# Performance work log

Hardware: AMD Instinct MI355X
Metric: run time of the kernel (lower is better)

## Reference

```python
import jax, jax.numpy as jnp
import numpy as np

DIM = 1024
DIM_HEAD = 64
HEADS = 16
NUM_LATENTS = 64
INNER = DIM_HEAD * HEADS  # 1024


def setup_inputs() -> dict:
    key = jax.random.key(0)
    ks = jax.random.split(key, 6)
    b, m, n = 8, 4, 1024
    x = jax.random.normal(ks[0], (b, m, n, DIM), dtype=jnp.float32)
    latents = jax.random.normal(ks[1], (NUM_LATENTS, DIM), dtype=jnp.float32)
    # Linear weights stored as (in, out); no bias for q/kv, bias for out (matches nn.Linear defaults)
    Wq = jax.random.normal(ks[2], (DIM, INNER), dtype=jnp.float32) * (DIM ** -0.5)
    Wkv = jax.random.normal(ks[3], (DIM, INNER * 2), dtype=jnp.float32) * (DIM ** -0.5)
    Wout = jax.random.normal(ks[4], (INNER, DIM), dtype=jnp.float32) * (INNER ** -0.5)
    bout = jax.random.normal(ks[5], (DIM,), dtype=jnp.float32) * 0.01
    return {"x": x, "latents": latents, "Wq": Wq, "Wkv": Wkv, "Wout": Wout, "bout": bout}


def reference(x, latents, Wq, Wkv, Wout, bout):
    b, m, n, d = x.shape
    h, dh = HEADS, DIM_HEAD
    scale = dh ** -0.5

    # q from latents: [n_lat, inner] -> [h, i, dh]
    q = (latents @ Wq).reshape(NUM_LATENTS, h, dh).transpose(1, 0, 2) * scale

    # k, v from media tokens: [b, m, n, 2*inner] -> two [b, h, m, n, dh]
    kv = x @ Wkv
    k, v = jnp.split(kv, 2, axis=-1)
    k = k.reshape(b, m, n, h, dh).transpose(0, 3, 1, 2, 4)  # b h m n dh
    v = v.reshape(b, m, n, h, dh).transpose(0, 3, 1, 2, 4)

    # latent k, v: [n_lat, 2*inner] -> [h, n_lat, dh] broadcast to [b, h, m, n_lat, dh]
    lkv = latents @ Wkv
    lk, lv = jnp.split(lkv, 2, axis=-1)
    lk = jnp.broadcast_to(lk.reshape(NUM_LATENTS, h, dh).transpose(1, 0, 2)[None, :, None], (b, h, m, NUM_LATENTS, dh))
    lv = jnp.broadcast_to(lv.reshape(NUM_LATENTS, h, dh).transpose(1, 0, 2)[None, :, None], (b, h, m, NUM_LATENTS, dh))

    k = jnp.concatenate((k, lk), axis=-2)  # b h m (n + n_lat) dh
    v = jnp.concatenate((v, lv), axis=-2)

    sim = jnp.einsum('hid,bhmjd->bhmij', q, k)
    attn = jax.nn.softmax(sim, axis=-1)  # stable softmax (max-subtract internal)
    out = jnp.einsum('bhmij,bhmjd->bhmid', attn, v)  # b h m i dh
    out = out.transpose(0, 2, 3, 1, 4).reshape(b, m, NUM_LATENTS, h * dh)  # b m i inner
    return out @ Wout + bout
```

## Files before the change

### kernel.cpp

```cpp
#include <hip/hip_runtime.h>
#include <cstdint>

typedef __attribute__((ext_vector_type(8))) __bf16 bf16x8;
typedef __attribute__((ext_vector_type(4))) float f32x4;
typedef __attribute__((ext_vector_type(8))) unsigned short u16x8;
typedef __attribute__((ext_vector_type(4))) unsigned short u16x4;

__device__ __forceinline__ unsigned short f2bf(float f) {
    union { float f; unsigned u; } v; v.f = f;
    unsigned u = v.u;
    return (unsigned short)((u + 0x7FFFu + ((u >> 16) & 1u)) >> 16);
}

__device__ __forceinline__ void gload_lds16(const void* g, void* l) {
    auto gp = reinterpret_cast<__attribute__((address_space(1))) unsigned*>(
        reinterpret_cast<uintptr_t>(g));
    auto lp = reinterpret_cast<__attribute__((address_space(3))) unsigned*>(
        reinterpret_cast<uintptr_t>(l));
    __builtin_amdgcn_global_load_lds(gp, lp, 16, 0, 0);
}

__global__ __launch_bounds__(256) void cvt_kernel(const float* __restrict__ in,
                                                  unsigned short* __restrict__ out, int n4) {
    int idx = blockIdx.x * 256 + threadIdx.x;
    int stride = gridDim.x * 256;
    for (int i = idx; i < n4; i += stride) {
        float4 v = ((const float4*)in)[i];
        u16x4 o;
        o.x = f2bf(v.x); o.y = f2bf(v.y); o.z = f2bf(v.z); o.w = f2bf(v.w);
        ((u16x4*)out)[i] = o;
    }
}

__global__ __launch_bounds__(256) void transpose_cvt(const float* __restrict__ in,
                                                     unsigned short* __restrict__ out,
                                                     int R, int C) {
    __shared__ float t[32][33];
    int c0 = blockIdx.x * 32, r0 = blockIdx.y * 32;
    int tx = threadIdx.x, ty = threadIdx.y;
    for (int i = ty; i < 32; i += 8)
        t[i][tx] = in[(size_t)(r0 + i) * C + c0 + tx];
    __syncthreads();
    for (int i = ty; i < 32; i += 8)
        out[(size_t)(c0 + i) * R + r0 + tx] = f2bf(t[tx][i]);
}

__global__ __launch_bounds__(256) void gemm128p(const unsigned short* __restrict__ A,
                                                const unsigned short* __restrict__ Bt,
                                                void* __restrict__ C,
                                                const float* __restrict__ bias,
                                                int M, int N, int K, float scale, int split,
                                                int c_f32) {
    __shared__ unsigned short lds[3][2][4096];
    int ntx = N >> 7;
    int nwg = gridDim.x, bid = blockIdx.x, swz = bid;
    if ((nwg & 7) == 0) { int cpx = nwg >> 3; swz = (bid & 7) * cpx + (bid >> 3); }
    int m0 = (swz / ntx) << 7, n0 = (swz % ntx) << 7;
    int tid = threadIdx.x, lane = tid & 63, w = tid >> 6;
    int wm = w >> 1, wn = w & 1;
    int lr = lane & 15, lg = lane >> 4;
    int gq = lg ^ ((lr >> 1) & 3);
    int nkt = K >> 5;

    int arow = tid >> 2;
    int sgl = (tid & 3) ^ ((arow >> 1) & 3);
    int ra0 = m0 + arow;      if (ra0 > M - 1) ra0 = M - 1;
    int ra1 = m0 + 64 + arow; if (ra1 > M - 1) ra1 = M - 1;
    const unsigned short* a0 = A + (size_t)ra0 * K + (sgl << 3);
    const unsigned short* a1 = A + (size_t)ra1 * K + (sgl << 3);
    const unsigned short* b0 = Bt + (size_t)(n0 + arow) * K + (sgl << 3);
    const unsigned short* b1 = Bt + (size_t)(n0 + 64 + arow) * K + (sgl << 3);

    f32x4 acc[4][4] = {};

#define ST_A128(bi, kt) do { \
        gload_lds16(a0 + ((kt) << 5), &lds[bi][0][w << 9]); \
        gload_lds16(a1 + ((kt) << 5), &lds[bi][0][2048 + (w << 9)]); } while (0)
#define ST_B128(bi, kt) do { \
        gload_lds16(b0 + ((kt) << 5), &lds[bi][1][w << 9]); \
        gload_lds16(b1 + ((kt) << 5), &lds[bi][1][2048 + (w << 9)]); } while (0)

    ST_A128(0, 0); ST_B128(0, 0);
    ST_A128(1, 1); ST_B128(1, 1);

    int buf = 0;
    for (int t = 0; t < nkt; ++t) {
        asm volatile("s_waitcnt vmcnt(4)" ::: "memory");
        __builtin_amdgcn_s_barrier();
        int st = t + 2; if (st >= nkt) st = nkt - 1;
        int sbuf = buf + 2; if (sbuf >= 3) sbuf -= 3;
        ST_A128(sbuf, st);
        ST_B128(sbuf, st);
        const unsigned short* pa = &lds[buf][0][((wm << 6) + lr) * 32 + (gq << 3)];
        const unsigned short* pb = &lds[buf][1][((wn << 6) + lr) * 32 + (gq << 3)];
        bf16x8 af[4], bfr[4];
#pragma unroll
        for (int nt = 0; nt < 4; nt++) bfr[nt] = *(const bf16x8*)(pb + nt * 512);
#pragma unroll
        for (int mt = 0; mt < 4; mt++) af[mt] = *(const bf16x8*)(pa + mt * 512);
        __builtin_amdgcn_s_barrier();
        __builtin_amdgcn_s_setprio(1);
#pragma unroll
        for (int mt = 0; mt < 4; mt++)
#pragma unroll
            for (int nt = 0; nt < 4; nt++)
                acc[mt][nt] = __builtin_amdgcn_mfma_f32_16x16x32_bf16(af[mt], bfr[nt], acc[mt][nt], 0, 0, 0);
        __builtin_amdgcn_s_setprio(0);
        buf++; if (buf == 3) buf = 0;
    }
#undef ST_A128
#undef ST_B128

#pragma unroll
    for (int mt = 0; mt < 4; mt++) {
#pragma unroll
        for (int nt = 0; nt < 4; nt++) {
            int col = n0 + (wn << 6) + (nt << 4) + lr;
            float sc = (col < split) ? scale : 1.0f;
            float bv = bias ? bias[col] : 0.0f;
#pragma unroll
            for (int r = 0; r < 4; r++) {
                int row = m0 + (wm << 6) + (mt << 4) + (lg << 2) + r;
                if (row < M) {
                    float v = acc[mt][nt][r] * sc + bv;
                    if (c_f32) ((float*)C)[(size_t)row * N + col] = v;
                    else       ((unsigned short*)C)[(size_t)row * N + col] = f2bf(v);
                }
            }
        }
    }
}

__global__ __launch_bounds__(512, 2) void gemm256(const unsigned short* __restrict__ A,
                                                  const unsigned short* __restrict__ Bt,
                                                  unsigned short* __restrict__ C,
                                                  int M, int N, int K) {
    __shared__ unsigned short lds[3][2][8192];
    int nkt = K >> 5;
    int ntx = N >> 8;
    int nwg = gridDim.x, bid = blockIdx.x, swz = bid;
    if ((nwg & 7) == 0) { int cpx = nwg >> 3; swz = (bid & 7) * cpx + (bid >> 3); }
    int m0 = (swz / ntx) << 8, n0 = (swz % ntx) << 8;
    int tid = threadIdx.x, lane = tid & 63, w = tid >> 6;
    int wm = w >> 2, wn = w & 3;
    int lr = lane & 15, lg = lane >> 4;
    int gq = lg ^ ((lr >> 1) & 3);

    int srow = tid >> 2;
    int sgl = (tid & 3) ^ ((srow >> 1) & 3);
    const unsigned short* a0 = A + (size_t)(m0 + srow) * K + (sgl << 3);
    const unsigned short* a1 = A + (size_t)(m0 + 128 + srow) * K + (sgl << 3);
    const unsigned short* b0 = Bt + (size_t)(n0 + srow) * K + (sgl << 3);
    const unsigned short* b1 = Bt + (size_t)(n0 + 128 + srow) * K + (sgl << 3);

    f32x4 acc[8][4] = {};

#define STAGE_A256(bufi, kt) do { \
        gload_lds16(a0 + ((kt) << 5), &lds[bufi][0][w << 9]); \
        gload_lds16(a1 + ((kt) << 5), &lds[bufi][0][4096 + (w << 9)]); } while (0)
#define STAGE_B256(bufi, kt) do { \
        gload_lds16(b0 + ((kt) << 5), &lds[bufi][1][w << 9]); \
        gload_lds16(b1 + ((kt) << 5), &lds[bufi][1][4096 + (w << 9)]); } while (0)

    STAGE_A256(0, 0); STAGE_B256(0, 0);
    STAGE_A256(1, 1); STAGE_B256(1, 1);

    int buf = 0;
    for (int t = 0; t < nkt; ++t) {
        asm volatile("s_waitcnt vmcnt(4)" ::: "memory");
        __builtin_amdgcn_s_barrier();
        int st = t + 2; if (st >= nkt) st = nkt - 1;
        int sbuf = buf + 2; if (sbuf >= 3) sbuf -= 3;

        const unsigned short* pa = &lds[buf][0][((wm << 7) + lr) * 32 + (gq << 3)];
        const unsigned short* pb = &lds[buf][1][((wn << 6) + lr) * 32 + (gq << 3)];

        STAGE_A256(sbuf, st);
        bf16x8 bfr[4], af[4];
#pragma unroll
        for (int nt = 0; nt < 4; nt++) bfr[nt] = *(const bf16x8*)(pb + nt * 512);
#pragma unroll
        for (int mt = 0; mt < 4; mt++) af[mt] = *(const bf16x8*)(pa + mt * 512);
        __builtin_amdgcn_s_barrier();
        __builtin_amdgcn_s_setprio(1);
#pragma unroll
        for (int mt = 0; mt < 4; mt++)
#pragma unroll
            for (int nt = 0; nt < 4; nt++)
                acc[mt][nt] = __builtin_amdgcn_mfma_f32_16x16x32_bf16(af[mt], bfr[nt], acc[mt][nt], 0, 0, 0);
        __builtin_amdgcn_s_setprio(0);
        __builtin_amdgcn_s_barrier();

        STAGE_B256(sbuf, st);
        bf16x8 ag[4];
#pragma unroll
        for (int mt = 0; mt < 4; mt++) ag[mt] = *(const bf16x8*)(pa + (mt + 4) * 512);
        __builtin_amdgcn_s_barrier();
        __builtin_amdgcn_s_setprio(1);
#pragma unroll
        for (int mt = 0; mt < 4; mt++)
#pragma unroll
            for (int nt = 0; nt < 4; nt++)
                acc[mt + 4][nt] = __builtin_amdgcn_mfma_f32_16x16x32_bf16(ag[mt], bfr[nt], acc[mt + 4][nt], 0, 0, 0);
        __builtin_amdgcn_s_setprio(0);

        buf++; if (buf == 3) buf = 0;
    }
#undef STAGE_A256
#undef STAGE_B256

#pragma unroll
    for (int mt = 0; mt < 8; mt++) {
#pragma unroll
        for (int nt = 0; nt < 4; nt++) {
            int col = n0 + (wn << 6) + (nt << 4) + lr;
            size_t rbase = (size_t)(m0 + (wm << 7) + (mt << 4) + (lg << 2));
#pragma unroll
            for (int r = 0; r < 4; r++)
                C[(rbase + r) * N + col] = f2bf(acc[mt][nt][r]);
        }
    }
}

__global__ __launch_bounds__(256) void attn_kernel(const unsigned short* __restrict__ qg, int qstride,
                                                   const unsigned short* __restrict__ kvg,
                                                   const unsigned short* __restrict__ lkvg, int lstride,
                                                   unsigned short* __restrict__ og) {
    __shared__ unsigned short K_lds[64 * 72];
    __shared__ unsigned short V_lds[64 * 72];
    __shared__ unsigned short P_lds[4][16 * 72];
    int bm = blockIdx.x >> 4, h = blockIdx.x & 15;
    int tid = threadIdx.x, lane = tid & 63, w = tid >> 6;
    int lr = lane & 15, lg = lane >> 4;

    bf16x8 qf[2];
#pragma unroll
    for (int kk = 0; kk < 2; kk++)
        qf[kk] = *(const bf16x8*)(qg + (size_t)((w << 4) + lr) * qstride + (h << 6) + (kk << 5) + (lg << 3));

    f32x4 acc[4] = {};
    float m_run[4], l_run[4];
#pragma unroll
    for (int r = 0; r < 4; r++) { m_run[r] = -1e30f; l_run[r] = 0.0f; }

    int jrow = tid >> 2;
    int seg = (tid & 3) << 4;

    const unsigned short* s0 = kvg + (size_t)((bm << 10) + jrow) * 2048 + (h << 6);
    u16x8 k0 = *(const u16x8*)(s0 + seg);
    u16x8 k1 = *(const u16x8*)(s0 + seg + 8);
    u16x8 v0 = *(const u16x8*)(s0 + 1024 + seg);
    u16x8 v1 = *(const u16x8*)(s0 + 1024 + seg + 8);

    for (int t = 0; t < 17; t++) {
        *(u16x8*)(&K_lds[jrow * 72 + seg]) = k0;
        *(u16x8*)(&K_lds[jrow * 72 + seg + 8]) = k1;
#pragma unroll
        for (int c = 0; c < 8; c++) V_lds[(seg + c) * 72 + jrow] = v0[c];
#pragma unroll
        for (int c = 0; c < 8; c++) V_lds[(seg + 8 + c) * 72 + jrow] = v1[c];
        __syncthreads();

        u16x8 nk0 = k0, nk1 = k1, nv0 = v0, nv1 = v1;
        if (t < 16) {
            const unsigned short* src = (t < 15)
                ? kvg + (size_t)((bm << 10) + ((t + 1) << 6) + jrow) * 2048 + (h << 6)
                : lkvg + (size_t)jrow * lstride + (h << 6);
            nk0 = *(const u16x8*)(src + seg);
            nk1 = *(const u16x8*)(src + seg + 8);
            nv0 = *(const u16x8*)(src + 1024 + seg);
            nv1 = *(const u16x8*)(src + 1024 + seg + 8);
        }

        f32x4 s[4] = {};
#pragma unroll
        for (int jt = 0; jt < 4; jt++) {
#pragma unroll
            for (int kk = 0; kk < 2; kk++) {
                bf16x8 kf = *(const bf16x8*)(&K_lds[(size_t)((jt << 4) + lr) * 72 + (kk << 5) + (lg << 3)]);
                s[jt] = __builtin_amdgcn_mfma_f32_16x16x32_bf16(qf[kk], kf, s[jt], 0, 0, 0);
            }
        }
#pragma unroll
        for (int r = 0; r < 4; r++) {
            float mx = fmaxf(fmaxf(s[0][r], s[1][r]), fmaxf(s[2][r], s[3][r]));
            mx = fmaxf(mx, __shfl_xor(mx, 1));
            mx = fmaxf(mx, __shfl_xor(mx, 2));
            mx = fmaxf(mx, __shfl_xor(mx, 4));
            mx = fmaxf(mx, __shfl_xor(mx, 8));
            float nm = fmaxf(m_run[r], mx);
            float fct = __expf(m_run[r] - nm);
            m_run[r] = nm;
            float p0 = __expf(s[0][r] - nm);
            float p1 = __expf(s[1][r] - nm);
            float p2 = __expf(s[2][r] - nm);
            float p3 = __expf(s[3][r] - nm);
            float sum = p0 + p1 + p2 + p3;
            sum += __shfl_xor(sum, 1);
            sum += __shfl_xor(sum, 2);
            sum += __shfl_xor(sum, 4);
            sum += __shfl_xor(sum, 8);
            l_run[r] = l_run[r] * fct + sum;
#pragma unroll
            for (int dt = 0; dt < 4; dt++) acc[dt][r] *= fct;
            int prow = ((lg << 2) + r) * 72;
            P_lds[w][prow + lr]      = f2bf(p0);
            P_lds[w][prow + 16 + lr] = f2bf(p1);
            P_lds[w][prow + 32 + lr] = f2bf(p2);
            P_lds[w][prow + 48 + lr] = f2bf(p3);
        }
#pragma unroll
        for (int jkk = 0; jkk < 2; jkk++) {
            bf16x8 pf = *(const bf16x8*)(&P_lds[w][(size_t)lr * 72 + (jkk << 5) + (lg << 3)]);
#pragma unroll
            for (int dt = 0; dt < 4; dt++) {
                bf16x8 vf = *(const bf16x8*)(&V_lds[(size_t)((dt << 4) + lr) * 72 + (jkk << 5) + (lg << 3)]);
                acc[dt] = __builtin_amdgcn_mfma_f32_16x16x32_bf16(pf, vf, acc[dt], 0, 0, 0);
            }
        }
        __syncthreads();
        k0 = nk0; k1 = nk1; v0 = nv0; v1 = nv1;
    }
#pragma unroll
    for (int dt = 0; dt < 4; dt++) {
#pragma unroll
        for (int r = 0; r < 4; r++) {
            int i = (w << 4) + (lg << 2) + r;
            float v = acc[dt][r] / l_run[r];
            og[(size_t)((bm << 6) + i) * 1024 + (h << 6) + (dt << 4) + lr] = f2bf(v);
        }
    }
}

extern "C" void kernel_launch(void* const* d_in, const int* in_sizes, int n_in,
                              void* d_out, int out_size, void* d_ws, size_t ws_size,
                              hipStream_t stream) {
    const float* x       = (const float*)d_in[0];
    const float* latents = (const float*)d_in[1];
    const float* Wq      = (const float*)d_in[2];
    const float* Wkv     = (const float*)d_in[3];
    const float* Wout    = (const float*)d_in[4];
    const float* bout    = (const float*)d_in[5];
    char* ws = (char*)d_ws;
    unsigned short* xb    = (unsigned short*)(ws);
    unsigned short* kvb   = (unsigned short*)(ws + 67108864);
    unsigned short* wqkvt = (unsigned short*)(ws + 201326592);
    unsigned short* wkvt  = wqkvt + 1024 * 1024;
    unsigned short* woutt = (unsigned short*)(ws + 207618048);
    unsigned short* latb  = (unsigned short*)(ws + 209715200);
    unsigned short* qlkvb = (unsigned short*)(ws + 209846272);
    unsigned short* attnb = (unsigned short*)(ws + 210239488);

    cvt_kernel<<<2048, 256, 0, stream>>>(x, xb, 33554432 / 4);
    cvt_kernel<<<64, 256, 0, stream>>>(latents, latb, 65536 / 4);
    dim3 tb(32, 8);
    transpose_cvt<<<dim3(32, 32), tb, 0, stream>>>(Wq, wqkvt, 1024, 1024);
    transpose_cvt<<<dim3(64, 32), tb, 0, stream>>>(Wkv, wkvt, 1024, 2048);
    transpose_cvt<<<dim3(32, 32), tb, 0, stream>>>(Wout, woutt, 1024, 1024);
    gemm128p<<<24, 256, 0, stream>>>(latb, wqkvt, qlkvb, nullptr, 64, 3072, 1024, 0.125f, 1024, 0);
    gemm256<<<1024, 512, 0, stream>>>(xb, wkvt, kvb, 32768, 2048, 1024);
    attn_kernel<<<512, 256, 0, stream>>>(qlkvb, 3072, kvb, qlkvb + 1024, 3072, attnb);
    gemm128p<<<128, 256, 0, stream>>>(attnb, woutt, (void*)d_out, bout, 2048, 1024, 1024, 1.0f, 0, 1);
}
```

Baseline: 271.0 us.

## Enlarge KV projection GEMM tile to 512x256 with 128x128 per-wave tiles

Replaces the 256x256-tile KV projection GEMM with a 512x256 tile in which each of the 8 waves computes a 128x128 sub-tile, halving the grid to 512 workgroups. The aim is more reuse of each LDS fragment per MFMA and less global traffic per output. The intermediate barriers inside the K loop are dropped in this kernel and one is also removed from gemm128p. In exchange, the doubled accumulator array (64 f32x4 per thread) under launch_bounds(512,2) is likely to exceed the register budget and spill. The larger triple-buffered LDS footprint also limits occupancy to one block per CU.

```diff
diff --git a/kernel.cpp b/kernel.cpp
--- a/kernel.cpp
+++ b/kernel.cpp
@@ -98,7 +98,6 @@
         for (int nt = 0; nt < 4; nt++) bfr[nt] = *(const bf16x8*)(pb + nt * 512);
 #pragma unroll
         for (int mt = 0; mt < 4; mt++) af[mt] = *(const bf16x8*)(pa + mt * 512);
-        __builtin_amdgcn_s_barrier();
         __builtin_amdgcn_s_setprio(1);
 #pragma unroll
         for (int mt = 0; mt < 4; mt++)
@@ -131,89 +130,86 @@
     }
 }
 
-__global__ __launch_bounds__(512, 2) void gemm256(const unsigned short* __restrict__ A,
+__global__ __launch_bounds__(512, 2) void gemm512(const unsigned short* __restrict__ A,
                                                   const unsigned short* __restrict__ Bt,
                                                   unsigned short* __restrict__ C,
                                                   int M, int N, int K) {
-    __shared__ unsigned short lds[3][2][8192];
+    __shared__ unsigned short lds[3][24576];
     int nkt = K >> 5;
     int ntx = N >> 8;
     int nwg = gridDim.x, bid = blockIdx.x, swz = bid;
     if ((nwg & 7) == 0) { int cpx = nwg >> 3; swz = (bid & 7) * cpx + (bid >> 3); }
-    int m0 = (swz / ntx) << 8, n0 = (swz % ntx) << 8;
+    int m0 = (swz / ntx) << 9, n0 = (swz % ntx) << 8;
     int tid = threadIdx.x, lane = tid & 63, w = tid >> 6;
-    int wm = w >> 2, wn = w & 3;
+    int wm = w >> 1, wn = w & 1;
     int lr = lane & 15, lg = lane >> 4;
     int gq = lg ^ ((lr >> 1) & 3);
 
     int srow = tid >> 2;
     int sgl = (tid & 3) ^ ((srow >> 1) & 3);
-    const unsigned short* a0 = A + (size_t)(m0 + srow) * K + (sgl << 3);
-    const unsigned short* a1 = A + (size_t)(m0 + 128 + srow) * K + (sgl << 3);
-    const unsigned short* b0 = Bt + (size_t)(n0 + srow) * K + (sgl << 3);
-    const unsigned short* b1 = Bt + (size_t)(n0 + 128 + srow) * K + (sgl << 3);
-
-    f32x4 acc[8][4] = {};
-
-#define STAGE_A256(bufi, kt) do { \
-        gload_lds16(a0 + ((kt) << 5), &lds[bufi][0][w << 9]); \
-        gload_lds16(a1 + ((kt) << 5), &lds[bufi][0][4096 + (w << 9)]); } while (0)
-#define STAGE_B256(bufi, kt) do { \
-        gload_lds16(b0 + ((kt) << 5), &lds[bufi][1][w << 9]); \
-        gload_lds16(b1 + ((kt) << 5), &lds[bufi][1][4096 + (w << 9)]); } while (0)
-
-    STAGE_A256(0, 0); STAGE_B256(0, 0);
-    STAGE_A256(1, 1); STAGE_B256(1, 1);
+    const unsigned short* aP = A + (size_t)(m0 + srow) * K + (sgl << 3);
+    const unsigned short* bP = Bt + (size_t)(n0 + srow) * K + (sgl << 3);
+    size_t aStep = (size_t)128 * K;
+
+    f32x4 acc[8][8] = {};
+
+#define ST_P1(bi, kt) do { \
+        gload_lds16(aP + ((kt) << 5),             &lds[bi][(w << 9)]); \
+        gload_lds16(aP + aStep + ((kt) << 5),     &lds[bi][4096 + (w << 9)]); \
+        gload_lds16(aP + 2 * aStep + ((kt) << 5), &lds[bi][8192 + (w << 9)]); } while (0)
+#define ST_P2(bi, kt) do { \
+        gload_lds16(aP + 3 * aStep + ((kt) << 5), &lds[bi][12288 + (w << 9)]); \
+        gload_lds16(bP + ((kt) << 5),             &lds[bi][16384 + (w << 9)]); \
+        gload_lds16(bP + aStep + ((kt) << 5),     &lds[bi][20480 + (w << 9)]); } while (0)
+
+    ST_P1(0, 0); ST_P2(0, 0);
+    ST_P1(1, 1); ST_P2(1, 1);
 
     int buf = 0;
     for (int t = 0; t < nkt; ++t) {
-        asm volatile("s_waitcnt vmcnt(4)" ::: "memory");
+        asm volatile("s_waitcnt vmcnt(6)" ::: "memory");
         __builtin_amdgcn_s_barrier();
         int st = t + 2; if (st >= nkt) st = nkt - 1;
         int sbuf = buf + 2; if (sbuf >= 3) sbuf -= 3;
 
-        const unsigned short* pa = &lds[buf][0][((wm << 7) + lr) * 32 + (gq << 3)];
-        const unsigned short* pb = &lds[buf][1][((wn << 6) + lr) * 32 + (gq << 3)];
-
-        STAGE_A256(sbuf, st);
-        bf16x8 bfr[4], af[4];
+        const unsigned short* pa = &lds[buf][((wm << 7) + lr) * 32 + (gq << 3)];
+        const unsigned short* pb = &lds[buf][16384 + ((wn << 7) + lr) * 32 + (gq << 3)];
+
+        ST_P1(sbuf, st);
+        bf16x8 af[8], bfr[4];
+#pragma unroll
+        for (int mt = 0; mt < 8; mt++) af[mt] = *(const bf16x8*)(pa + mt * 512);
 #pragma unroll
         for (int nt = 0; nt < 4; nt++) bfr[nt] = *(const bf16x8*)(pb + nt * 512);
-#pragma unroll
-        for (int mt = 0; mt < 4; mt++) af[mt] = *(const bf16x8*)(pa + mt * 512);
-        __builtin_amdgcn_s_barrier();
         __builtin_amdgcn_s_setprio(1);
 #pragma unroll
-        for (int mt = 0; mt < 4; mt++)
+        for (int mt = 0; mt < 8; mt++)
 #pragma unroll
             for (int nt = 0; nt < 4; nt++)
                 acc[mt][nt] = __builtin_amdgcn_mfma_f32_16x16x32_bf16(af[mt], bfr[nt], acc[mt][nt], 0, 0, 0);
         __builtin_amdgcn_s_setprio(0);
-        __builtin_amdgcn_s_barrier();
-
-        STAGE_B256(sbuf, st);
-        bf16x8 ag[4];
-#pragma unroll
-        for (int mt = 0; mt < 4; mt++) ag[mt] = *(const bf16x8*)(pa + (mt + 4) * 512);
-        __builtin_amdgcn_s_barrier();
+
+        ST_P2(sbuf, st);
+#pragma unroll
+        for (int nt = 0; nt < 4; nt++) bfr[nt] = *(const bf16x8*)(pb + (nt + 4) * 512);
         __builtin_amdgcn_s_setprio(1);
 #pragma unroll
-        for (int mt = 0; mt < 4; mt++)
+        for (int mt = 0; mt < 8; mt++)
 #pragma unroll
             for (int nt = 0; nt < 4; nt++)
-                acc[mt + 4][nt] = __builtin_amdgcn_mfma_f32_16x16x32_bf16(ag[mt], bfr[nt], acc[mt + 4][nt], 0, 0, 0);
+                acc[mt][nt + 4] = __builtin_amdgcn_mfma_f32_16x16x32_bf16(af[mt], bfr[nt], acc[mt][nt + 4], 0, 0, 0);
         __builtin_amdgcn_s_setprio(0);
 
         buf++; if (buf == 3) buf = 0;
     }
-#undef STAGE_A256
-#undef STAGE_B256
+#undef ST_P1
+#undef ST_P2
 
 #pragma unroll
     for (int mt = 0; mt < 8; mt++) {
 #pragma unroll
-        for (int nt = 0; nt < 4; nt++) {
-            int col = n0 + (wn << 6) + (nt << 4) + lr;
+        for (int nt = 0; nt < 8; nt++) {
+            int col = n0 + (wn << 7) + (nt << 4) + lr;
             size_t rbase = (size_t)(m0 + (wm << 7) + (mt << 4) + (lg << 2));
 #pragma unroll
             for (int r = 0; r < 4; r++)
@@ -358,7 +354,7 @@
     transpose_cvt<<<dim3(64, 32), tb, 0, stream>>>(Wkv, wkvt, 1024, 2048);
     transpose_cvt<<<dim3(32, 32), tb, 0, stream>>>(Wout, woutt, 1024, 1024);
     gemm128p<<<24, 256, 0, stream>>>(latb, wqkvt, qlkvb, nullptr, 64, 3072, 1024, 0.125f, 1024, 0);
-    gemm256<<<1024, 512, 0, stream>>>(xb, wkvt, kvb, 32768, 2048, 1024);
+    gemm512<<<512, 512, 0, stream>>>(xb, wkvt, kvb, 32768, 2048, 1024);
     attn_kernel<<<512, 256, 0, stream>>>(qlkvb, 3072, kvb, qlkvb + 1024, 3072, attnb);
     gemm128p<<<128, 256, 0, stream>>>(attnb, woutt, (void*)d_out, bout, 2048, 1024, 1024, 1.0f, 0, 1);
 }
```

Measured after the change: 974.2 us. 259% more time.

## Load A operand directly into registers in gemm256 and drop redundant barriers

Applied to the files above, without the earlier changes.

The 256x256 GEMM stops staging the A tile through LDS. Each wave now loads its own A fragments straight from global memory into registers one k-step ahead, while B stays triple-buffered in LDS. This removes the A LDS traffic and two of the three per-iteration barriers, and the 128 GEMM also loses one barrier in favour of an lgkmcnt wait. In exchange there are more VGPRs, uncoalesced 16-byte global loads for A that are not shared between waves, and global load latency exposed to each wave directly.

```diff
diff --git a/kernel.cpp b/kernel.cpp
--- a/kernel.cpp
+++ b/kernel.cpp
@@ -85,8 +85,10 @@
 
     int buf = 0;
     for (int t = 0; t < nkt; ++t) {
-        asm volatile("s_waitcnt vmcnt(4)" ::: "memory");
+        asm volatile("s_waitcnt vmcnt(4) lgkmcnt(0)" ::: "memory");
+        __builtin_amdgcn_sched_barrier(0);
         __builtin_amdgcn_s_barrier();
+        __builtin_amdgcn_sched_barrier(0);
         int st = t + 2; if (st >= nkt) st = nkt - 1;
         int sbuf = buf + 2; if (sbuf >= 3) sbuf -= 3;
         ST_A128(sbuf, st);
@@ -98,7 +100,6 @@
         for (int nt = 0; nt < 4; nt++) bfr[nt] = *(const bf16x8*)(pb + nt * 512);
 #pragma unroll
         for (int mt = 0; mt < 4; mt++) af[mt] = *(const bf16x8*)(pa + mt * 512);
-        __builtin_amdgcn_s_barrier();
         __builtin_amdgcn_s_setprio(1);
 #pragma unroll
         for (int mt = 0; mt < 4; mt++)
@@ -135,7 +136,7 @@
                                                   const unsigned short* __restrict__ Bt,
                                                   unsigned short* __restrict__ C,
                                                   int M, int N, int K) {
-    __shared__ unsigned short lds[3][2][8192];
+    __shared__ unsigned short ldsB[3][8192];
     int nkt = K >> 5;
     int ntx = N >> 8;
     int nwg = gridDim.x, bid = blockIdx.x, swz = bid;
@@ -148,66 +149,67 @@
 
     int srow = tid >> 2;
     int sgl = (tid & 3) ^ ((srow >> 1) & 3);
-    const unsigned short* a0 = A + (size_t)(m0 + srow) * K + (sgl << 3);
-    const unsigned short* a1 = A + (size_t)(m0 + 128 + srow) * K + (sgl << 3);
     const unsigned short* b0 = Bt + (size_t)(n0 + srow) * K + (sgl << 3);
     const unsigned short* b1 = Bt + (size_t)(n0 + 128 + srow) * K + (sgl << 3);
 
+    const unsigned short* aBase = A + (size_t)(m0 + (wm << 7) + lr) * K + (lg << 3);
+    size_t aRowStep = (size_t)16 * K;
+
     f32x4 acc[8][4] = {};
-
-#define STAGE_A256(bufi, kt) do { \
-        gload_lds16(a0 + ((kt) << 5), &lds[bufi][0][w << 9]); \
-        gload_lds16(a1 + ((kt) << 5), &lds[bufi][0][4096 + (w << 9)]); } while (0)
-#define STAGE_B256(bufi, kt) do { \
-        gload_lds16(b0 + ((kt) << 5), &lds[bufi][1][w << 9]); \
-        gload_lds16(b1 + ((kt) << 5), &lds[bufi][1][4096 + (w << 9)]); } while (0)
-
-    STAGE_A256(0, 0); STAGE_B256(0, 0);
-    STAGE_A256(1, 1); STAGE_B256(1, 1);
+    bf16x8 areg[8];
+
+#define ST_B(bi, kt) do { \
+        gload_lds16(b0 + ((kt) << 5), &ldsB[bi][w << 9]); \
+        gload_lds16(b1 + ((kt) << 5), &ldsB[bi][4096 + (w << 9)]); } while (0)
+#define LD_A(mt_, kt) areg[mt_] = *(const bf16x8*)(aBase + (size_t)(mt_) * aRowStep + ((kt) << 5))
+
+#pragma unroll
+    for (int mt = 0; mt < 8; mt++) LD_A(mt, 0);
+    __builtin_amdgcn_sched_barrier(0);
+    ST_B(0, 0);
+    ST_B(1, 1);
 
     int buf = 0;
     for (int t = 0; t < nkt; ++t) {
-        asm volatile("s_waitcnt vmcnt(4)" ::: "memory");
+        asm volatile("s_waitcnt vmcnt(2) lgkmcnt(0)" ::: "memory");
+        __builtin_amdgcn_sched_barrier(0);
         __builtin_amdgcn_s_barrier();
-        int st = t + 2; if (st >= nkt) st = nkt - 1;
+        __builtin_amdgcn_sched_barrier(0);
+        int tn = t + 1; if (tn >= nkt) tn = nkt - 1;
+        int ts = t + 2; if (ts >= nkt) ts = nkt - 1;
         int sbuf = buf + 2; if (sbuf >= 3) sbuf -= 3;
 
-        const unsigned short* pa = &lds[buf][0][((wm << 7) + lr) * 32 + (gq << 3)];
-        const unsigned short* pb = &lds[buf][1][((wn << 6) + lr) * 32 + (gq << 3)];
-
-        STAGE_A256(sbuf, st);
-        bf16x8 bfr[4], af[4];
+        const unsigned short* pb = &ldsB[buf][((wn << 6) + lr) * 32 + (gq << 3)];
+        bf16x8 bfr[4];
 #pragma unroll
         for (int nt = 0; nt < 4; nt++) bfr[nt] = *(const bf16x8*)(pb + nt * 512);
-#pragma unroll
-        for (int mt = 0; mt < 4; mt++) af[mt] = *(const bf16x8*)(pa + mt * 512);
-        __builtin_amdgcn_s_barrier();
+
         __builtin_amdgcn_s_setprio(1);
 #pragma unroll
         for (int mt = 0; mt < 4; mt++)
 #pragma unroll
             for (int nt = 0; nt < 4; nt++)
-                acc[mt][nt] = __builtin_amdgcn_mfma_f32_16x16x32_bf16(af[mt], bfr[nt], acc[mt][nt], 0, 0, 0);
+                acc[mt][nt] = __builtin_amdgcn_mfma_f32_16x16x32_bf16(areg[mt], bfr[nt], acc[mt][nt], 0, 0, 0);
         __builtin_amdgcn_s_setprio(0);
-        __builtin_amdgcn_s_barrier();
-
-        STAGE_B256(sbuf, st);
-        bf16x8 ag[4];
-#pragma unroll
-        for (int mt = 0; mt < 4; mt++) ag[mt] = *(const bf16x8*)(pa + (mt + 4) * 512);
-        __builtin_amdgcn_s_barrier();
+#pragma unroll
+        for (int mt = 0; mt < 4; mt++) LD_A(mt, tn);
+
         __builtin_amdgcn_s_setprio(1);
 #pragma unroll
-        for (int mt = 0; mt < 4; mt++)
+        for (int mt = 4; mt < 8; mt++)
 #pragma unroll
             for (int nt = 0; nt < 4; nt++)
-                acc[mt + 4][nt] = __builtin_amdgcn_mfma_f32_16x16x32_bf16(ag[mt], bfr[nt], acc[mt + 4][nt], 0, 0, 0);
+                acc[mt][nt] = __builtin_amdgcn_mfma_f32_16x16x32_bf16(areg[mt], bfr[nt], acc[mt][nt], 0, 0, 0);
         __builtin_amdgcn_s_setprio(0);
+#pragma unroll
+        for (int mt = 4; mt < 8; mt++) LD_A(mt, tn);
+        __builtin_amdgcn_sched_barrier(0);
+        ST_B(sbuf, ts);
 
         buf++; if (buf == 3) buf = 0;
     }
-#undef STAGE_A256
-#undef STAGE_B256
+#undef ST_B
+#undef LD_A
 
 #pragma unroll
     for (int mt = 0; mt < 8; mt++) {
```

Result: slower. 442.7 us (+63.3%).
